# Kernel tuning notes

Hardware: AMD Instinct MI355X
Metric: run time of the kernel (lower is better)

Reference implementation:

```python
import jax, jax.numpy as jnp
import numpy as np

M, N, D, P, N_kv = 512, 4096, 128, 3584, 1024
H, H_kv = N // D, N_kv // D          # 32 query heads, 8 kv heads
G = H // H_kv                        # group size 4
L = P + M                            # cache length 4096


def setup_inputs() -> dict:
    key = jax.random.key(0)
    ks = jax.random.split(key, 6)
    w_scale = 0.008  # ~0.5/sqrt(N): keeps unscaled exp-softmax logits in fp32 range
    return {
        "X": jax.random.normal(ks[0], (M, N), jnp.float32),
        "W_q": jax.random.normal(ks[1], (N, N), jnp.float32) * w_scale,
        "W_k": jax.random.normal(ks[2], (N, N_kv), jnp.float32) * w_scale,
        "W_v": jax.random.normal(ks[3], (N, N_kv), jnp.float32) * w_scale,
        "cache_K": jax.random.normal(ks[4], (H, L, D), jnp.float32) * 0.02,
        "cache_V": jax.random.normal(ks[5], (H, L, D), jnp.float32) * 0.02,
    }


def reference(X, W_q, W_k, W_v, cache_K, cache_V):
    # fused QKV projection
    W_qkv = jnp.concatenate([W_q, W_k, W_v], axis=1)        # [N, N + 2*N_kv]
    qkv = X @ W_qkv                                          # [M, N + 2*N_kv]
    q = qkv[:, :N].reshape(M, H, D).transpose(1, 0, 2)       # [H, M, D]
    k = qkv[:, N:N + N_kv].reshape(M, H_kv, D).transpose(1, 0, 2)   # [H_kv, M, D]
    v = qkv[:, N + N_kv:].reshape(M, H_kv, D).transpose(1, 0, 2)    # [H_kv, M, D]
    # expand grouped KV heads (repeat_interleave) and append to cache at P
    k_exp = jnp.repeat(k, G, axis=0)                         # [H, M, D]
    v_exp = jnp.repeat(v, G, axis=0)
    Kc = cache_K.at[:, P:P + M, :].set(k_exp)                # [H, L, D]
    Vc = cache_V.at[:, P:P + M, :].set(v_exp)
    # naive (unscaled, non-max-subtracted) softmax attention over full cache
    scores = jnp.einsum('hmd,hld->hml', q, Kc)               # [H, M, L]
    e = jnp.exp(scores)
    weights = e / jnp.sum(e, axis=-1, keepdims=True)
    out = jnp.einsum('hml,hld->hmd', weights, Vc)            # [H, M, D]
    return out.transpose(1, 0, 2).reshape(M, H * D)          # [M, N]
```

## Files before the change

kernel.cpp:

```cpp
#include <hip/hip_runtime.h>

typedef __attribute__((ext_vector_type(8))) short short8;
typedef __attribute__((ext_vector_type(4))) float f32x4;

#define M_   512
#define N_   4096
#define D_   128
#define P_   3584
#define NKV  1024
#define L_   4096
#define H_   32

__device__ __forceinline__ ushort f2bf(float f) {
  union { float f; unsigned u; } v; v.f = f;
  unsigned r = (v.u + 0x7fffu + ((v.u >> 16) & 1u)) >> 16;
  return (ushort)r;
}
__device__ __forceinline__ float bf2f(ushort u) {
  union { unsigned u; float f; } v; v.u = ((unsigned)u) << 16;
  return v.f;
}

__device__ __forceinline__ void gload_lds16(const void* g, void* l) {
  __builtin_amdgcn_global_load_lds(
      (const __attribute__((address_space(1))) void*)g,
      (__attribute__((address_space(3))) void*)l, 16, 0, 0);
}

__global__ __launch_bounds__(256) void xconv(const float* __restrict__ X,
                                             ushort* __restrict__ Xs)
{
  int g = blockIdx.x * 256 + threadIdx.x;
  int row = g >> 9;
  int cir = g & 511;
  int grp = cir >> 3, ch = cir & 7;
  const float* src = &X[(size_t)row * 4096 + cir * 8];
  float4 f0 = *reinterpret_cast<const float4*>(src);
  float4 f1 = *reinterpret_cast<const float4*>(src + 4);
  short8 s;
  s[0] = f2bf(f0.x); s[1] = f2bf(f0.y); s[2] = f2bf(f0.z); s[3] = f2bf(f0.w);
  s[4] = f2bf(f1.x); s[5] = f2bf(f1.y); s[6] = f2bf(f1.z); s[7] = f2bf(f1.w);
  int dcol = grp * 64 + ((ch ^ (row & 7)) * 8);
  *reinterpret_cast<short8*>(&Xs[(size_t)row * 4096 + dcol]) = s;
}

__global__ __launch_bounds__(256) void wtrans(
    const float* __restrict__ Wq, const float* __restrict__ Wk,
    const float* __restrict__ Wv, ushort* __restrict__ Wt)
{
  int bx = blockIdx.x;
  int by = blockIdx.y;
  const float* W; int wcols, c0;
  if (by < 64)      { W = Wq; wcols = 4096; c0 = by * 64; }
  else if (by < 80) { W = Wk; wcols = 1024; c0 = (by - 64) * 64; }
  else              { W = Wv; wcols = 1024; c0 = (by - 80) * 64; }
  int orow0 = by * 64;
  int r0 = bx * 64;
  __shared__ float T[64][65];
  int tid = threadIdx.x;

  #pragma unroll
  for (int i = 0; i < 4; ++i) {
    int r = i * 16 + (tid >> 4);
    int c4 = tid & 15;
    float4 f = *reinterpret_cast<const float4*>(&W[(size_t)(r0 + r) * wcols + c0 + c4 * 4]);
    T[r][c4 * 4 + 0] = f.x; T[r][c4 * 4 + 1] = f.y;
    T[r][c4 * 4 + 2] = f.z; T[r][c4 * 4 + 3] = f.w;
  }
  __syncthreads();

  #pragma unroll
  for (int i = 0; i < 2; ++i) {
    int j = i * 256 + tid;
    int orr = j >> 3;
    int ch = j & 7;
    short8 s;
    #pragma unroll
    for (int e = 0; e < 8; ++e) s[e] = f2bf(T[ch * 8 + e][orr]);
    int orow = orow0 + orr;
    int dstch = ch ^ (orow & 7);
    *reinterpret_cast<short8*>(&Wt[(size_t)orow * 4096 + r0 + dstch * 8]) = s;
  }
}

#define GEMM_STAGE(buf, k0g) do {                                             \
    _Pragma("unroll")                                                         \
    for (int i_ = 0; i_ < 4; ++i_) {                                          \
      int blk_ = w * 4 + i_;                                                  \
      gload_lds16(Asrc + (size_t)(blk_ * 8 + (lane >> 3)) * 4096 + (k0g) + (lane & 7) * 8, \
                  &As[buf][blk_ * 512]);                                      \
    }                                                                         \
    _Pragma("unroll")                                                         \
    for (int i_ = 0; i_ < 4; ++i_) {                                          \
      int blk_ = w * 4 + i_;                                                  \
      gload_lds16(Bsrc + (size_t)(blk_ * 8 + (lane >> 3)) * 4096 + (k0g) + (lane & 7) * 8, \
                  &Bs[buf][blk_ * 512]);                                      \
    }                                                                         \
  } while (0)

__global__ __launch_bounds__(256, 2) void qkv_gemm3(
    const ushort* __restrict__ Xs, const ushort* __restrict__ Wt,
    float* __restrict__ pg)
{
  const int bx = blockIdx.x;
  const int by = blockIdx.y;
  const int bz = blockIdx.z;
  const int tid = threadIdx.x, lane = tid & 63, w = tid >> 6;
  const int wr = w >> 1, wc = w & 1;
  const int m0 = by * 128, n0 = bx * 128;
  const int kb0 = bz * 2048;

  __shared__ ushort As[2][128 * 64];
  __shared__ ushort Bs[2][128 * 64];

  f32x4 acc[4][4];
  #pragma unroll
  for (int m = 0; m < 4; ++m)
    #pragma unroll
    for (int n = 0; n < 4; ++n)
      acc[m][n] = (f32x4){0.f, 0.f, 0.f, 0.f};

  const ushort* Asrc = Xs + (size_t)m0 * 4096;
  const ushort* Bsrc = Wt + (size_t)n0 * 4096;

  GEMM_STAGE(0, kb0);
  __syncthreads();
  int cur = 0;

  for (int kt = 0; kt < 32; ++kt) {
    if (kt + 1 < 32) GEMM_STAGE(cur ^ 1, kb0 + (kt + 1) * 64);
    #pragma unroll
    for (int kk = 0; kk < 2; ++kk) {
      short8 a[4], b[4];
      #pragma unroll
      for (int m = 0; m < 4; ++m) {
        int row = wr * 64 + m * 16 + (lane & 15);
        int ch = (kk * 4 + (lane >> 4)) ^ (row & 7);
        a[m] = *reinterpret_cast<const short8*>(&As[cur][row * 64 + ch * 8]);
      }
      #pragma unroll
      for (int n = 0; n < 4; ++n) {
        int row = wc * 64 + n * 16 + (lane & 15);
        int ch = (kk * 4 + (lane >> 4)) ^ (row & 7);
        b[n] = *reinterpret_cast<const short8*>(&Bs[cur][row * 64 + ch * 8]);
      }
      #pragma unroll
      for (int m = 0; m < 4; ++m)
        #pragma unroll
        for (int n = 0; n < 4; ++n)
          acc[m][n] = __builtin_amdgcn_mfma_f32_16x16x32_bf16(a[m], b[n], acc[m][n], 0, 0, 0);
    }
    __syncthreads();
    cur ^= 1;
  }

  float* dst = pg + (size_t)bz * 512 * 6144;
  #pragma unroll
  for (int m = 0; m < 4; ++m)
    #pragma unroll
    for (int n = 0; n < 4; ++n)
      #pragma unroll
      for (int j = 0; j < 4; ++j) {
        int row = m0 + wr * 64 + m * 16 + (lane >> 4) * 4 + j;
        int col = n0 + wc * 64 + n * 16 + (lane & 15);
        dst[(size_t)row * 6144 + col] = acc[m][n][j];
      }
}

__global__ __launch_bounds__(256) void combine_qk(
    const float* __restrict__ pg, ushort* __restrict__ qb,
    ushort* __restrict__ Kbn)
{
  int id = blockIdx.x * 256 + threadIdx.x;
  int m = id / 640;
  int c8 = (id - m * 640) * 8;
  const float* p0 = pg + (size_t)m * 6144 + c8;
  const float* p1 = p0 + (size_t)512 * 6144;
  short8 s;
  #pragma unroll
  for (int e = 0; e < 8; ++e) s[e] = f2bf(p0[e] + p1[e]);
  if (c8 < 4096) {
    *reinterpret_cast<short8*>(&qb[(size_t)m * 4096 + c8]) = s;
  } else {
    int o = c8 - 4096;
    int hk = o >> 7, d0 = o & 127;
    #pragma unroll
    for (int g = 0; g < 4; ++g)
      *reinterpret_cast<short8*>(&Kbn[((size_t)(hk * 4 + g) * 512 + m) * 128 + d0]) = s;
  }
}

__global__ __launch_bounds__(256) void combine_v(
    const float* __restrict__ pg, ushort* __restrict__ Vtn)
{
  int bz = blockIdx.x;
  int mt = bz & 7, hk = (bz >> 3) & 7, dh = bz >> 6;
  int m0 = mt * 64;
  int d0 = dh * 64;
  int colbase = 5120 + hk * 128 + d0;
  __shared__ float T[64][65];
  int tid = threadIdx.x;
  int r = tid >> 2, q4 = tid & 3;

  #pragma unroll
  for (int i = 0; i < 4; ++i) {
    int c = (q4 * 4 + i) * 4;
    const float* p0 = pg + (size_t)(m0 + r) * 6144 + colbase + c;
    const float* p1 = p0 + (size_t)512 * 6144;
    float4 a = *reinterpret_cast<const float4*>(p0);
    float4 b = *reinterpret_cast<const float4*>(p1);
    T[r][c + 0] = a.x + b.x; T[r][c + 1] = a.y + b.y;
    T[r][c + 2] = a.z + b.z; T[r][c + 3] = a.w + b.w;
  }
  __syncthreads();

  #pragma unroll
  for (int p = 0; p < 2; ++p) {
    int idx = p * 256 + tid;
    int dloc = idx >> 3, cc = idx & 7;
    int half = cc >> 2, c4 = (cc & 3) * 4;
    short8 s;
    #pragma unroll
    for (int e = 0; e < 8; ++e) {
      int lrow = half * 32 + c4 + (e < 4 ? e : 16 + (e - 4));
      s[e] = f2bf(T[lrow][dloc]);
    }
    int d = d0 + dloc;
    #pragma unroll
    for (int g = 0; g < 4; ++g) {
      int h = hk * 4 + g;
      *reinterpret_cast<short8*>(&Vtn[((size_t)h * 128 + d) * 512 + m0 + cc * 8]) = s;
    }
  }
}

#define ATTN_TILE(bufc) do {                                                  \
    const ushort* Ksb = &Ks[bufc][0];                                         \
    const ushort* Vsb = &Vt[bufc][0];                                         \
    f32x4 sc0 = (f32x4){0.f, 0.f, 0.f, 0.f};                                  \
    f32x4 sc1 = (f32x4){0.f, 0.f, 0.f, 0.f};                                  \
    __builtin_amdgcn_s_setprio(1);                                            \
    _Pragma("unroll")                                                         \
    for (int kk = 0; kk < 4; ++kk) {                                          \
      int ch = (kk * 4 + hi) ^ (lo16 & 7);                                    \
      short8 a0 = *reinterpret_cast<const short8*>(&Ksb[lo16 * 128 + ch * 8]); \
      short8 a1 = *reinterpret_cast<const short8*>(&Ksb[(16 + lo16) * 128 + ch * 8]); \
      sc0 = __builtin_amdgcn_mfma_f32_16x16x32_bf16(a0, qreg[kk], sc0, 0, 0, 0); \
      sc1 = __builtin_amdgcn_mfma_f32_16x16x32_bf16(a1, qreg[kk], sc1, 0, 0, 0); \
    }                                                                         \
    __builtin_amdgcn_s_setprio(0);                                            \
    short8 pa;                                                                \
    {                                                                         \
      float e0 = __expf(sc0[0]); float e1 = __expf(sc0[1]);                   \
      float e2 = __expf(sc0[2]); float e3 = __expf(sc0[3]);                   \
      float f0 = __expf(sc1[0]); float f1 = __expf(sc1[1]);                   \
      float f2 = __expf(sc1[2]); float f3 = __expf(sc1[3]);                   \
      rs += ((e0 + e1) + (e2 + e3)) + ((f0 + f1) + (f2 + f3));                \
      pa[0] = f2bf(e0); pa[1] = f2bf(e1); pa[2] = f2bf(e2); pa[3] = f2bf(e3); \
      pa[4] = f2bf(f0); pa[5] = f2bf(f1); pa[6] = f2bf(f2); pa[7] = f2bf(f3); \
    }                                                                         \
    __builtin_amdgcn_s_setprio(1);                                            \
    _Pragma("unroll")                                                         \
    for (int n = 0; n < 8; ++n) {                                             \
      int d = n * 16 + lo16;                                                  \
      int chv = hi ^ ((d >> 1) & 3);                                          \
      short8 bn = *reinterpret_cast<const short8*>(&Vsb[d * 32 + chv * 8]);   \
      o[n] = __builtin_amdgcn_mfma_f32_16x16x32_bf16(pa, bn, o[n], 0, 0, 0);  \
    }                                                                         \
    __builtin_amdgcn_s_setprio(0);                                            \
  } while (0)

#define AISSUE(t_) do {                                                       \
    if (s3 && (t_) >= 16) {                                                   \
      krn = *reinterpret_cast<const short8*>(                                 \
          &KsrcN[(size_t)((t_) * 32 - 512 + klr) * 128 + kc * 8]);            \
      vrn = *reinterpret_cast<const short8*>(                                 \
          &VsrcN[(size_t)vd * 512 + ((t_) * 32 - 512) + vc3 * 8]);            \
    } else {                                                                  \
      const float* kp_ = &Ksrc[(size_t)((t_) * 32 + klr) * 128 + kc * 8];     \
      kr0 = *reinterpret_cast<const float4*>(kp_);                            \
      kr1 = *reinterpret_cast<const float4*>(kp_ + 4);                        \
      _Pragma("unroll")                                                       \
      for (int e_ = 0; e_ < 8; ++e_) {                                        \
        int lr_ = (t_) * 32 + vc3 * 4 + (e_ < 4 ? e_ : 16 + (e_ - 4));        \
        vr[e_] = Vsrc[(size_t)lr_ * 128 + vd];                                \
      }                                                                       \
    }                                                                         \
  } while (0)

#define AWRITE(t_) do {                                                       \
    short8 ks_, vs_;                                                          \
    if (s3 && (t_) >= 16) { ks_ = krn; vs_ = vrn; }                           \
    else {                                                                    \
      ks_[0] = f2bf(kr0.x); ks_[1] = f2bf(kr0.y);                             \
      ks_[2] = f2bf(kr0.z); ks_[3] = f2bf(kr0.w);                             \
      ks_[4] = f2bf(kr1.x); ks_[5] = f2bf(kr1.y);                             \
      ks_[6] = f2bf(kr1.z); ks_[7] = f2bf(kr1.w);                             \
      _Pragma("unroll")                                                       \
      for (int e_ = 0; e_ < 8; ++e_) vs_[e_] = f2bf(vr[e_]);                  \
    }                                                                         \
    *reinterpret_cast<short8*>(&Ks[(t_) & 3][klr * 128 + ((kc ^ (klr & 7)) * 8)]) = ks_; \
    *reinterpret_cast<short8*>(&Vt[(t_) & 3][vd * 32 + (((vc3 ^ (vd >> 1)) & 3) * 8)]) = vs_; \
  } while (0)

__global__ __launch_bounds__(512, 4) void gqa_attn12(
    const ushort* __restrict__ qb, const float* __restrict__ cacheK,
    const float* __restrict__ cacheV, const ushort* __restrict__ Kbn,
    const ushort* __restrict__ Vtn,
    ushort* __restrict__ pob, float* __restrict__ prs)
{
  const int b = blockIdx.x;
  const int s = b & 3;
  const int j = b >> 2;
  const int qt = j & 3;
  const int h = j >> 2;
  const int tid = threadIdx.x, lane = tid & 63, w = tid >> 6;
  const int lo16 = lane & 15, hi = lane >> 4;

  __shared__ ushort Ks[4][32 * 128];
  __shared__ ushort Vt[4][128 * 32];

  short8 qreg[4];
  {
    int qrow = qt * 128 + w * 16 + lo16;
    #pragma unroll
    for (int kk = 0; kk < 4; ++kk)
      qreg[kk] = *reinterpret_cast<const short8*>(
          &qb[(size_t)qrow * 4096 + h * 128 + (kk * 4 + hi) * 8]);
  }

  f32x4 o[8];
  #pragma unroll
  for (int n = 0; n < 8; ++n)
    o[n] = (f32x4){0.f, 0.f, 0.f, 0.f};
  float rs = 0.f;

  const int klr = tid >> 4, kc = tid & 15;
  const int vd = tid >> 2, vc3 = tid & 3;
  const float* Ksrc = cacheK + ((size_t)h * L_ + s * 1024) * 128;
  const float* Vsrc = cacheV + ((size_t)h * L_ + s * 1024) * 128;
  const ushort* KsrcN = Kbn + (size_t)h * 512 * 128;
  const ushort* VsrcN = Vtn + (size_t)h * 128 * 512;
  const bool s3 = (s == 3);

  float4 kr0, kr1;
  float vr[8];
  short8 krn, vrn;

  AISSUE(0);
  AWRITE(0);
  AISSUE(1);
  asm volatile("s_waitcnt lgkmcnt(0)" ::: "memory");
  __builtin_amdgcn_s_barrier();

  for (int t = 0; t < 32; ++t) {
    if (t + 1 < 32) AWRITE(t + 1);
    if (t + 2 < 32) AISSUE(t + 2);
    ATTN_TILE(t & 3);
    asm volatile("s_waitcnt lgkmcnt(0)" ::: "memory");
    __builtin_amdgcn_s_barrier();
  }

  float rsum = rs;
  rsum += __shfl_xor(rsum, 16, 64);
  rsum += __shfl_xor(rsum, 32, 64);

  const size_t pbase = (size_t)(s * 32 + h) * 512;
  #pragma unroll
  for (int n = 0; n < 8; ++n)
    #pragma unroll
    for (int j2 = 0; j2 < 4; ++j2) {
      int row = qt * 128 + w * 16 + hi * 4 + j2;
      pob[(pbase + row) * 128 + n * 16 + lo16] = f2bf(o[n][j2]);
    }
  if (hi == 0) {
    int row = qt * 128 + w * 16 + lo16;
    prs[pbase + row] = rsum;
  }
}

__global__ __launch_bounds__(256) void reduce_out(
    const ushort* __restrict__ pob, const float* __restrict__ prs,
    float* __restrict__ out)
{
  int id = blockIdx.x * 256 + threadIdx.x;
  int m = id >> 10, dq = id & 1023;
  int h = dq >> 5, d4 = dq & 31;
  float4 acc = {0.f, 0.f, 0.f, 0.f};
  float rsum = 0.f;
  #pragma unroll
  for (int s = 0; s < 4; ++s) {
    size_t base = (size_t)(s * 32 + h) * 512 + m;
    ushort4 v = *reinterpret_cast<const ushort4*>(&pob[base * 128 + d4 * 4]);
    acc.x += bf2f(v.x); acc.y += bf2f(v.y); acc.z += bf2f(v.z); acc.w += bf2f(v.w);
    rsum += prs[base];
  }
  float inv = 1.f / rsum;
  float4 r; r.x = acc.x * inv; r.y = acc.y * inv; r.z = acc.z * inv; r.w = acc.w * inv;
  *reinterpret_cast<float4*>(&out[(size_t)m * 4096 + dq * 4]) = r;
}

extern "C" void kernel_launch(void* const* d_in, const int* in_sizes, int n_in,
                              void* d_out, int out_size, void* d_ws, size_t ws_size,
                              hipStream_t stream) {
  const float* X  = (const float*)d_in[0];
  const float* Wq = (const float*)d_in[1];
  const float* Wk = (const float*)d_in[2];
  const float* Wv = (const float*)d_in[3];
  const float* cK = (const float*)d_in[4];
  const float* cV = (const float*)d_in[5];
  float* out = (float*)d_out;

  ushort* qb  = (ushort*)d_ws;
  ushort* Xs  = qb  + (size_t)M_ * N_;
  ushort* Kbn = Xs  + (size_t)M_ * N_;
  ushort* Vtn = Kbn + (size_t)H_ * 512 * D_;
  float*  prs = (float*)(Vtn + (size_t)H_ * 512 * D_);
  ushort* pob = (ushort*)(prs + 8 * 32 * 512);
  ushort* Wt  = pob + (size_t)4 * H_ * 512 * D_;
  float*  pg  = (float*)(Wt + (size_t)6144 * 4096);

  xconv<<<1024, 256, 0, stream>>>(X, Xs);
  wtrans<<<dim3(64, 96), 256, 0, stream>>>(Wq, Wk, Wv, Wt);
  qkv_gemm3<<<dim3(48, 4, 2), 256, 0, stream>>>(Xs, Wt, pg);
  combine_qk<<<1280, 256, 0, stream>>>(pg, qb, Kbn);
  combine_v<<<128, 256, 0, stream>>>(pg, Vtn);
  gqa_attn12<<<512, 512, 0, stream>>>(qb, cK, cV, Kbn, Vtn, pob, prs);
  reduce_out<<<2048, 256, 0, stream>>>(pob, prs, out);
}
```

Before: 169.7 us.

## Pre-transpose cached V to bf16 in a separate kernel before attention

Adds a vconv kernel that converts the fp32 V cache prefix into a transposed bf16 buffer of full cache length. combine_v now writes the new V into the same buffer at offset P. The attention kernel then reads V with one uniform short8 load per tile instead of eight strided fp32 scalar loads plus conversion. This trades an extra kernel launch and an extra pass over V (read fp32, write bf16) for coalesced, half-width V reads inside the attention loop.

```diff
diff --git a/kernel.cpp b/kernel.cpp
--- a/kernel.cpp
+++ b/kernel.cpp
@@ -229,8 +229,43 @@
     #pragma unroll
     for (int g = 0; g < 4; ++g) {
       int h = hk * 4 + g;
-      *reinterpret_cast<short8*>(&Vtn[((size_t)h * 128 + d) * 512 + m0 + cc * 8]) = s;
+      *reinterpret_cast<short8*>(&Vtn[((size_t)h * 128 + d) * (size_t)L_ + P_ + m0 + cc * 8]) = s;
     }
+  }
+}
+
+__global__ __launch_bounds__(256) void vconv(
+    const float* __restrict__ cacheV, ushort* __restrict__ Vtn)
+{
+  int h = blockIdx.x, lt = blockIdx.y, dh = blockIdx.z;
+  int l0 = lt * 64, d0 = dh * 64;
+  __shared__ float T[64][65];
+  int tid = threadIdx.x;
+  int r4 = tid >> 4, c = tid & 15;
+
+  #pragma unroll
+  for (int p = 0; p < 4; ++p) {
+    int r = p * 16 + r4;
+    float4 f = *reinterpret_cast<const float4*>(
+        &cacheV[((size_t)h * L_ + l0 + r) * 128 + d0 + c * 4]);
+    T[r][c * 4 + 0] = f.x; T[r][c * 4 + 1] = f.y;
+    T[r][c * 4 + 2] = f.z; T[r][c * 4 + 3] = f.w;
+  }
+  __syncthreads();
+
+  int dr = tid >> 2, part = tid & 3;
+  int d = d0 + dr;
+  #pragma unroll
+  for (int q = 0; q < 2; ++q) {
+    int cc = part * 2 + q;
+    int half = cc >> 2, c4 = (cc & 3) * 4;
+    short8 s;
+    #pragma unroll
+    for (int e = 0; e < 8; ++e) {
+      int lrow = half * 32 + c4 + (e < 4 ? e : 16 + (e - 4));
+      s[e] = f2bf(T[lrow][dr]);
+    }
+    *reinterpret_cast<short8*>(&Vtn[((size_t)h * 128 + d) * (size_t)L_ + l0 + cc * 8]) = s;
   }
 }
 
@@ -274,39 +309,31 @@
     if (s3 && (t_) >= 16) {                                                   \
       krn = *reinterpret_cast<const short8*>(                                 \
           &KsrcN[(size_t)((t_) * 32 - 512 + klr) * 128 + kc * 8]);            \
-      vrn = *reinterpret_cast<const short8*>(                                 \
-          &VsrcN[(size_t)vd * 512 + ((t_) * 32 - 512) + vc3 * 8]);            \
     } else {                                                                  \
       const float* kp_ = &Ksrc[(size_t)((t_) * 32 + klr) * 128 + kc * 8];     \
       kr0 = *reinterpret_cast<const float4*>(kp_);                            \
       kr1 = *reinterpret_cast<const float4*>(kp_ + 4);                        \
-      _Pragma("unroll")                                                       \
-      for (int e_ = 0; e_ < 8; ++e_) {                                        \
-        int lr_ = (t_) * 32 + vc3 * 4 + (e_ < 4 ? e_ : 16 + (e_ - 4));        \
-        vr[e_] = Vsrc[(size_t)lr_ * 128 + vd];                                \
-      }                                                                       \
-    }                                                                         \
+    }                                                                         \
+    vrn = *reinterpret_cast<const short8*>(                                   \
+        &VsrcN[(size_t)vd * (size_t)L_ + (t_) * 32 + vc3 * 8]);               \
   } while (0)
 
 #define AWRITE(t_) do {                                                       \
-    short8 ks_, vs_;                                                          \
-    if (s3 && (t_) >= 16) { ks_ = krn; vs_ = vrn; }                           \
+    short8 ks_;                                                               \
+    if (s3 && (t_) >= 16) { ks_ = krn; }                                      \
     else {                                                                    \
       ks_[0] = f2bf(kr0.x); ks_[1] = f2bf(kr0.y);                             \
       ks_[2] = f2bf(kr0.z); ks_[3] = f2bf(kr0.w);                             \
       ks_[4] = f2bf(kr1.x); ks_[5] = f2bf(kr1.y);                             \
       ks_[6] = f2bf(kr1.z); ks_[7] = f2bf(kr1.w);                             \
-      _Pragma("unroll")                                                       \
-      for (int e_ = 0; e_ < 8; ++e_) vs_[e_] = f2bf(vr[e_]);                  \
     }                                                                         \
     *reinterpret_cast<short8*>(&Ks[(t_) & 3][klr * 128 + ((kc ^ (klr & 7)) * 8)]) = ks_; \
-    *reinterpret_cast<short8*>(&Vt[(t_) & 3][vd * 32 + (((vc3 ^ (vd >> 1)) & 3) * 8)]) = vs_; \
+    *reinterpret_cast<short8*>(&Vt[(t_) & 3][vd * 32 + (((vc3 ^ (vd >> 1)) & 3) * 8)]) = vrn; \
   } while (0)
 
-__global__ __launch_bounds__(512, 4) void gqa_attn12(
+__global__ __launch_bounds__(512, 4) void gqa_attn13(
     const ushort* __restrict__ qb, const float* __restrict__ cacheK,
-    const float* __restrict__ cacheV, const ushort* __restrict__ Kbn,
-    const ushort* __restrict__ Vtn,
+    const ushort* __restrict__ Kbn, const ushort* __restrict__ Vtn,
     ushort* __restrict__ pob, float* __restrict__ prs)
 {
   const int b = blockIdx.x;
@@ -338,13 +365,11 @@
   const int klr = tid >> 4, kc = tid & 15;
   const int vd = tid >> 2, vc3 = tid & 3;
   const float* Ksrc = cacheK + ((size_t)h * L_ + s * 1024) * 128;
-  const float* Vsrc = cacheV + ((size_t)h * L_ + s * 1024) * 128;
   const ushort* KsrcN = Kbn + (size_t)h * 512 * 128;
-  const ushort* VsrcN = Vtn + (size_t)h * 128 * 512;
+  const ushort* VsrcN = Vtn + (size_t)h * 128 * (size_t)L_ + s * 1024;
   const bool s3 = (s == 3);
 
   float4 kr0, kr1;
-  float vr[8];
   short8 krn, vrn;
 
   AISSUE(0);
@@ -415,7 +440,7 @@
   ushort* Xs  = qb  + (size_t)M_ * N_;
   ushort* Kbn = Xs  + (size_t)M_ * N_;
   ushort* Vtn = Kbn + (size_t)H_ * 512 * D_;
-  float*  prs = (float*)(Vtn + (size_t)H_ * 512 * D_);
+  float*  prs = (float*)(Vtn + (size_t)H_ * D_ * L_);
   ushort* pob = (ushort*)(prs + 8 * 32 * 512);
   ushort* Wt  = pob + (size_t)4 * H_ * 512 * D_;
   float*  pg  = (float*)(Wt + (size_t)6144 * 4096);
@@ -425,6 +450,7 @@
   qkv_gemm3<<<dim3(48, 4, 2), 256, 0, stream>>>(Xs, Wt, pg);
   combine_qk<<<1280, 256, 0, stream>>>(pg, qb, Kbn);
   combine_v<<<128, 256, 0, stream>>>(pg, Vtn);
-  gqa_attn12<<<512, 512, 0, stream>>>(qb, cK, cV, Kbn, Vtn, pob, prs);
+  vconv<<<dim3(32, 56, 2), 256, 0, stream>>>(cV, Vtn);
+  gqa_attn13<<<512, 512, 0, stream>>>(qb, cK, Kbn, Vtn, pob, prs);
   reduce_out<<<2048, 256, 0, stream>>>(pob, prs, out);
 }
```

Result: faster. 161.6 us (-4.8%).
